# Kernel tuning notes

Measured on AMD Instinct MI355X. Metric: run time of the kernel, lower is better.

Reference implementation:

```python
import jax, jax.numpy as jnp
import numpy as np
import math

D_MODEL = 1024
N_HEADS = 16
D_HEAD = 64
GROUP_SIZE = 2
N_GROUPS = N_HEADS // GROUP_SIZE
D_MLP = 4096
BATCH = 2
SEQ = 2048
LN_EPS = 1e-5


def setup_inputs() -> dict:
    key = jax.random.key(0)
    ks = jax.random.split(key, 12)

    def xavier(k, shape):
        # torch xavier_uniform on a 3D tensor treats dim0 as fan_in, prod(rest) as fan_out
        fan_in = shape[0]
        fan_out = int(np.prod(shape[1:]))
        bound = math.sqrt(6.0 / (fan_in + fan_out))
        return jax.random.uniform(k, shape, jnp.float32, -bound, bound)

    def linear_w(k, out_f, in_f):
        bound = 1.0 / math.sqrt(in_f)
        return jax.random.uniform(k, (out_f, in_f), jnp.float32, -bound, bound)

    return {
        "x": jax.random.normal(ks[0], (BATCH, SEQ, D_MODEL), jnp.float32),
        "ln1_w": jnp.ones((D_MODEL,), jnp.float32),
        "ln1_b": jnp.zeros((D_MODEL,), jnp.float32),
        "W_Q": xavier(ks[1], (D_MODEL, N_HEADS, D_HEAD)),
        "W_K": xavier(ks[2], (D_MODEL, N_GROUPS, D_HEAD)),
        "W_V": xavier(ks[3], (D_MODEL, N_GROUPS, D_HEAD)),
        "W_out": xavier(ks[4], (D_HEAD, N_HEADS, D_MODEL)),
        "b_out": jnp.zeros((D_MODEL,), jnp.float32),
        "ln2_w": jnp.ones((D_MODEL,), jnp.float32),
        "ln2_b": jnp.zeros((D_MODEL,), jnp.float32),
        "mlp1_w": linear_w(ks[5], D_MLP, D_MODEL),
        "mlp1_b": jax.random.uniform(ks[6], (D_MLP,), jnp.float32, -1.0 / math.sqrt(D_MODEL), 1.0 / math.sqrt(D_MODEL)),
        "mlp2_w": linear_w(ks[7], D_MODEL, D_MLP),
        "mlp2_b": jax.random.uniform(ks[8], (D_MODEL,), jnp.float32, -1.0 / math.sqrt(D_MLP), 1.0 / math.sqrt(D_MLP)),
    }


def _layernorm(x, w, b):
    mu = jnp.mean(x, axis=-1, keepdims=True)
    var = jnp.var(x, axis=-1, keepdims=True)
    return (x - mu) * jax.lax.rsqrt(var + LN_EPS) * w + b


def _gqa_attention(resid, W_Q, W_K, W_V, W_out, b_out):
    b, s, _ = resid.shape
    q = jnp.einsum("bsd,dhk->bshk", resid, W_Q)            # [b, s, n_heads, d_head]
    q = q.reshape(b, s, N_GROUPS, GROUP_SIZE, D_HEAD)      # [b, s, g, gs, k]
    k = jnp.einsum("bsd,dgk->bsgk", resid, W_K)            # [b, s, g, k]
    v = jnp.einsum("bsd,dgk->bsgk", resid, W_V)
    scores = jnp.einsum("bqgik,btgk->bgiqt", q, k) / math.sqrt(D_HEAD)  # [b, g, gs, q, t]
    causal_mask = jnp.triu(jnp.ones((s, s), dtype=bool), k=1)
    scores = jnp.where(causal_mask, jnp.float32(-1000000.0), scores)
    probs = jax.nn.softmax(scores, axis=-1)
    z = jnp.einsum("bgiqt,btgk->bqgik", probs, v)          # [b, q, g, gs, k]
    z = z.reshape(b, s, N_HEADS, D_HEAD)
    return jnp.einsum("bshk,khd->bsd", z, W_out) + b_out


def reference(x, ln1_w, ln1_b, W_Q, W_K, W_V, W_out, b_out,
              ln2_w, ln2_b, mlp1_w, mlp1_b, mlp2_w, mlp2_b):
    normed = _layernorm(x, ln1_w, ln1_b)
    attn_out = _gqa_attention(normed, W_Q, W_K, W_V, W_out, b_out)
    post_attn = x + attn_out
    h = _layernorm(post_attn, ln2_w, ln2_b)
    h = jax.nn.gelu(h @ mlp1_w.T + mlp1_b, approximate=False)  # torch nn.GELU default = exact erf
    mlp_out = h @ mlp2_w.T + mlp2_b
    return post_attn + mlp_out
```

## Files before the change

kernel.cpp:

```cpp
#include <hip/hip_runtime.h>
#include <cstdint>
#include <cstddef>

typedef __attribute__((ext_vector_type(8))) short short8;
typedef __attribute__((ext_vector_type(4))) float f32x4;
typedef unsigned short u16;

#define MFMA16(a, b, c) __builtin_amdgcn_mfma_f32_16x16x32_bf16((a), (b), (c), 0, 0, 0)
#define SCL2 0.18033688011112042f

__device__ __forceinline__ u16 f2bf(float f) {
  union { float f; unsigned u; } c; c.f = f;
  unsigned r = c.u + 0x7fffu + ((c.u >> 16) & 1u);
  return (u16)(r >> 16);
}

__device__ __forceinline__ float bf2f(u16 x) {
  union { unsigned u; float f; } c; c.u = ((unsigned)x) << 16;
  return c.f;
}

__device__ __forceinline__ unsigned cvtpk(float a, float b) {
  unsigned r;
  asm("v_cvt_pk_bf16_f32 %0, %1, %2" : "=v"(r) : "v"(a), "v"(b));
  return r;
}


__global__ __launch_bounds__(256) void prep_wqkv(const float* __restrict__ wq,
    const float* __restrict__ wk, const float* __restrict__ wv, u16* __restrict__ outp)
{
  __shared__ float t[32][33];
  const int tx = threadIdx.x & 31, ty = threadIdx.x >> 5;
  const int n0 = blockIdx.x * 32, d0 = blockIdx.y * 32;
  const float* src; int stride, nc;
  if (n0 < 1024)      { src = wq; stride = 1024; nc = n0; }
  else if (n0 < 1536) { src = wk; stride = 512;  nc = n0 - 1024; }
  else                { src = wv; stride = 512;  nc = n0 - 1536; }
#pragma unroll
  for (int i = 0; i < 32; i += 8)
    t[ty + i][tx] = src[(size_t)(d0 + ty + i) * stride + nc + tx];
  __syncthreads();
#pragma unroll
  for (int i = 0; i < 32; i += 8)
    outp[(size_t)(n0 + ty + i) * 1024 + d0 + tx] = f2bf(t[tx][ty + i]);
}

__global__ __launch_bounds__(256) void prep_wout(const float* __restrict__ wo, u16* __restrict__ outp)
{
  __shared__ float t[32][33];
  const int tx = threadIdx.x & 31, ty = threadIdx.x >> 5;
  const int d0 = blockIdx.x * 32, c0 = blockIdx.y * 32;
#pragma unroll
  for (int i = 0; i < 32; i += 8) {
    int c = c0 + ty + i;
    t[ty + i][tx] = wo[(size_t)(c & 63) * 16384 + (size_t)(c >> 6) * 1024 + d0 + tx];
  }
  __syncthreads();
#pragma unroll
  for (int i = 0; i < 32; i += 8)
    outp[(size_t)(d0 + ty + i) * 1024 + c0 + tx] = f2bf(t[tx][ty + i]);
}

__global__ void convert_bf16(const float4* __restrict__ in, u16* __restrict__ out, int n4) {
  int i = blockIdx.x * 256 + threadIdx.x;
  if (i >= n4) return;
  float4 v = in[i];
  ushort4 o; o.x = f2bf(v.x); o.y = f2bf(v.y); o.z = f2bf(v.z); o.w = f2bf(v.w);
  ((ushort4*)out)[i] = o;
}

__global__ __launch_bounds__(256) void vt_transpose(const u16* __restrict__ qkv, u16* __restrict__ vtp)
{
  __shared__ u16 t[32][33];
  const int tx = threadIdx.x & 31, ty = threadIdx.x >> 5;
  const int t0 = blockIdx.x * 32, k0 = blockIdx.y * 32;
  const int bg = blockIdx.z, b = bg >> 3, g = bg & 7;
#pragma unroll
  for (int i = 0; i < 32; i += 8)
    t[ty + i][tx] = qkv[(size_t)(b * 2048 + t0 + ty + i) * 2048 + 1536 + g * 64 + k0 + tx];
  __syncthreads();
#pragma unroll
  for (int i = 0; i < 32; i += 8)
    vtp[(size_t)(bg * 64 + k0 + ty + i) * 2048 + t0 + tx] = t[tx][ty + i];
}

__global__ __launch_bounds__(256) void ln_bf16(const float* __restrict__ x,
    const float* __restrict__ w, const float* __restrict__ b, u16* __restrict__ out)
{
  const int row = blockIdx.x, tid = threadIdx.x;
  const float4 v = ((const float4*)(x + (size_t)row * 1024))[tid];
  float s = v.x + v.y + v.z + v.w;
  float s2 = v.x * v.x + v.y * v.y + v.z * v.z + v.w * v.w;
#pragma unroll
  for (int m = 32; m >= 1; m >>= 1) { s += __shfl_xor(s, m); s2 += __shfl_xor(s2, m); }
  __shared__ float red[8];
  if ((tid & 63) == 0) { red[tid >> 6] = s; red[4 + (tid >> 6)] = s2; }
  __syncthreads();
  s  = red[0] + red[1] + red[2] + red[3];
  s2 = red[4] + red[5] + red[6] + red[7];
  const float mu = s * (1.f / 1024.f);
  const float inv = rsqrtf(s2 * (1.f / 1024.f) - mu * mu + 1e-5f);
  const float4 wv = ((const float4*)w)[tid];
  const float4 bv = ((const float4*)b)[tid];
  ushort4 o;
  o.x = f2bf((v.x - mu) * inv * wv.x + bv.x);
  o.y = f2bf((v.y - mu) * inv * wv.y + bv.y);
  o.z = f2bf((v.z - mu) * inv * wv.z + bv.z);
  o.w = f2bf((v.w - mu) * inv * wv.w + bv.w);
  ((ushort4*)out)[(size_t)row * 256 + tid] = o;
}

#define BM 128
#define BN 128
#define BK 32

template<int EPI>
__global__ __launch_bounds__(256, 2) void gemm_bt(
    const u16* __restrict__ A, const u16* __restrict__ Bt, void* __restrict__ Cout,
    const float* __restrict__ bias, const float* __restrict__ resid,
    int M, int N, int K)
{
  __shared__ u16 As[4][BM * BK];
  __shared__ u16 Bs[4][BN * BK];
  const int tid = threadIdx.x;
  const int w = tid >> 6, lane = tid & 63;
  const int lo = lane & 15, hi = lane >> 4;
  const int mBase = blockIdx.x * BM, nBase = blockIdx.y * BN;
  const int wr = (w >> 1) * 64, wc = (w & 1) * 64;

  const f32x4 vzero = {0.f, 0.f, 0.f, 0.f};
  f32x4 acc[4][4];
#pragma unroll
  for (int i = 0; i < 4; ++i)
#pragma unroll
    for (int j = 0; j < 4; ++j) acc[i][j] = vzero;

  const int base0 = w * 2048 + lane * 16;
  int srow[2], skb[2];
#pragma unroll
  for (int c = 0; c < 2; ++c) {
    const int off = base0 + c * 1024;
    srow[c] = off >> 6;
    skb[c] = ((off & 63) ^ ((srow[c] & 3) << 4)) >> 1;
  }

  const int NT = K >> 5;

  auto stage = [&](int kt) {
    const int slot = kt & 3;
    const int k0 = kt * BK;
#pragma unroll
    for (int c = 0; c < 2; ++c) {
      const u16* ga = A  + (size_t)(mBase + srow[c]) * K + k0 + skb[c];
      const u16* gb = Bt + (size_t)(nBase + srow[c]) * K + k0 + skb[c];
      __builtin_amdgcn_global_load_lds((const __attribute__((address_space(1))) void*)ga,
          (__attribute__((address_space(3))) void*)((char*)&As[slot][0] + w * 2048 + c * 1024), 16, 0, 0);
      __builtin_amdgcn_global_load_lds((const __attribute__((address_space(1))) void*)gb,
          (__attribute__((address_space(3))) void*)((char*)&Bs[slot][0] + w * 2048 + c * 1024), 16, 0, 0);
    }
  };

  stage(0);
  stage(1);

  for (int kt = 0; kt < NT; ++kt) {
    if (kt + 2 < NT) {
      stage(kt + 2);
      asm volatile("s_waitcnt vmcnt(8)" ::: "memory");
    } else if (kt + 1 < NT) {
      asm volatile("s_waitcnt vmcnt(4)" ::: "memory");
    } else {
      asm volatile("s_waitcnt vmcnt(0)" ::: "memory");
    }
    __builtin_amdgcn_s_barrier();
    __builtin_amdgcn_sched_barrier(0);

    const int slot = kt & 3;
    short8 af[4], bf[4];
#pragma unroll
    for (int i = 0; i < 4; ++i) {
      const int ra = wr + i * 16 + lo;
      const int rb = wc + i * 16 + lo;
      af[i] = *(const short8*)((const char*)&As[slot][0] + ra * 64 + ((hi * 16) ^ ((ra & 3) << 4)));
      bf[i] = *(const short8*)((const char*)&Bs[slot][0] + rb * 64 + ((hi * 16) ^ ((rb & 3) << 4)));
    }
    __builtin_amdgcn_s_setprio(1);
#pragma unroll
    for (int i = 0; i < 4; ++i)
#pragma unroll
      for (int j = 0; j < 4; ++j)
        acc[i][j] = MFMA16(af[i], bf[j], acc[i][j]);
    __builtin_amdgcn_s_setprio(0);
  }

#pragma unroll
  for (int i = 0; i < 4; ++i) {
#pragma unroll
    for (int j = 0; j < 4; ++j) {
#pragma unroll
      for (int r = 0; r < 4; ++r) {
        const int row = mBase + wr + i * 16 + hi * 4 + r;
        const int col = nBase + wc + j * 16 + lo;
        float v = acc[i][j][r];
        if (EPI == 3 && col < 1024) v *= SCL2;
        ((u16*)Cout)[(size_t)row * N + col] = f2bf(v);
      }
    }
  }
}

template<int EPI>
__global__ __launch_bounds__(256, 3) void gemm_n64(
    const u16* __restrict__ A, const u16* __restrict__ Bt, void* __restrict__ Cout,
    const float* __restrict__ bias, const float* __restrict__ resid,
    int M, int N, int K)
{
  __shared__ u16 As[4][128 * 32];
  __shared__ u16 Bs[4][64 * 32];
  const int tid = threadIdx.x;
  const int w = tid >> 6, lane = tid & 63;
  const int lo = lane & 15, hi = lane >> 4;
  const int mBase = blockIdx.x * 128, nBase = blockIdx.y * 64;
  const int wr = (w >> 1) * 64, wc = (w & 1) * 32;

  const f32x4 vzero = {0.f, 0.f, 0.f, 0.f};
  f32x4 acc[4][2];
#pragma unroll
  for (int i = 0; i < 4; ++i)
#pragma unroll
    for (int j = 0; j < 2; ++j) acc[i][j] = vzero;

  int arow[2], akb[2];
#pragma unroll
  for (int c = 0; c < 2; ++c) {
    const int off = tid * 16 + c * 4096;
    arow[c] = off >> 6;
    akb[c] = ((off & 63) ^ ((arow[c] & 3) << 4)) >> 1;
  }
  const int boff = tid * 16;
  const int brow = boff >> 6;
  const int bkb = ((boff & 63) ^ ((brow & 3) << 4)) >> 1;

  const int NT = K >> 5;

  auto stage = [&](int kt) {
    const int slot = kt & 3;
    const int k0 = kt * 32;
#pragma unroll
    for (int c = 0; c < 2; ++c) {
      const u16* ga = A + (size_t)(mBase + arow[c]) * K + k0 + akb[c];
      __builtin_amdgcn_global_load_lds((const __attribute__((address_space(1))) void*)ga,
          (__attribute__((address_space(3))) void*)((char*)&As[slot][0] + tid * 16 + c * 4096), 16, 0, 0);
    }
    const u16* gb = Bt + (size_t)(nBase + brow) * K + k0 + bkb;
    __builtin_amdgcn_global_load_lds((const __attribute__((address_space(1))) void*)gb,
        (__attribute__((address_space(3))) void*)((char*)&Bs[slot][0] + tid * 16), 16, 0, 0);
  };

  stage(0);
  stage(1);

  for (int kt = 0; kt < NT; ++kt) {
    if (kt + 2 < NT) {
      stage(kt + 2);
      asm volatile("s_waitcnt vmcnt(6)" ::: "memory");
    } else if (kt + 1 < NT) {
      asm volatile("s_waitcnt vmcnt(3)" ::: "memory");
    } else {
      asm volatile("s_waitcnt vmcnt(0)" ::: "memory");
    }
    __builtin_amdgcn_s_barrier();
    __builtin_amdgcn_sched_barrier(0);

    const int slot = kt & 3;
    short8 af[4], bf[2];
#pragma unroll
    for (int i = 0; i < 4; ++i) {
      const int ra = wr + i * 16 + lo;
      af[i] = *(const short8*)((const char*)&As[slot][0] + ra * 64 + ((hi * 16) ^ ((ra & 3) << 4)));
    }
#pragma unroll
    for (int j = 0; j < 2; ++j) {
      const int rb = wc + j * 16 + lo;
      bf[j] = *(const short8*)((const char*)&Bs[slot][0] + rb * 64 + ((hi * 16) ^ ((rb & 3) << 4)));
    }
    __builtin_amdgcn_s_setprio(1);
#pragma unroll
    for (int i = 0; i < 4; ++i)
#pragma unroll
      for (int j = 0; j < 2; ++j)
        acc[i][j] = MFMA16(af[i], bf[j], acc[i][j]);
    __builtin_amdgcn_s_setprio(0);
  }

#pragma unroll
  for (int i = 0; i < 4; ++i) {
#pragma unroll
    for (int j = 0; j < 2; ++j) {
#pragma unroll
      for (int r = 0; r < 4; ++r) {
        const int row = mBase + wr + i * 16 + hi * 4 + r;
        const int col = nBase + wc + j * 16 + lo;
        float v = acc[i][j][r];
        v += bias[col];
        v += resid[(size_t)row * N + col];
        ((float*)Cout)[(size_t)row * N + col] = v;
      }
    }
  }
}

template<int EPI>
__global__ __launch_bounds__(512, 2) void gemm256(
    const u16* __restrict__ A, const u16* __restrict__ Bt, void* __restrict__ Cout,
    const float* __restrict__ bias, const float* __restrict__ resid,
    int M, int N, int K)
{
  __shared__ u16 lds8[2][2][2][8192];
  const int tid = threadIdx.x;
  const int lane = tid & 63, lo = lane & 15, hi = lane >> 4;
  const int wid = tid >> 6, wr = wid >> 2, wc = wid & 3;
  const int mBase = blockIdx.x * 256, nBase = blockIdx.y * 256;
  const int sw = (lo & 7) << 4;

  const f32x4 vzero = {0.f, 0.f, 0.f, 0.f};
  f32x4 acc[8][4];
#pragma unroll
  for (int i = 0; i < 8; ++i)
#pragma unroll
    for (int j = 0; j < 4; ++j) acc[i][j] = vzero;

  int srow[2], scol[2];
#pragma unroll
  for (int c = 0; c < 2; ++c) {
    const int p = c * 8192 + tid * 16;
    const int r = p >> 7, bb = p & 127;
    srow[c] = r;
    scol[c] = (bb ^ ((r & 7) << 4)) >> 1;
  }

  const int NT = K >> 6;

#pragma unroll
  for (int mat = 0; mat < 2; ++mat)
#pragma unroll
    for (int half = 0; half < 2; ++half)
#pragma unroll
      for (int c = 0; c < 2; ++c) {
        const u16* g = (mat == 0)
          ? A  + (size_t)(mBase + half * 128 + srow[c]) * K + scol[c]
          : Bt + (size_t)(nBase + half * 128 + srow[c]) * K + scol[c];
        __builtin_amdgcn_global_load_lds((const __attribute__((address_space(1))) void*)g,
            (__attribute__((address_space(3))) void*)(&lds8[0][mat][half][c * 4096 + tid * 8]), 16, 0, 0);
      }
  asm volatile("s_waitcnt vmcnt(0)" ::: "memory");
  asm volatile("s_barrier" ::: "memory");

  for (int kt = 0; kt < NT; ++kt) {
    const int cur = kt & 1;
    const char* baseA = (const char*)&lds8[cur][0][wr][0];
    const char* baseB = (const char*)&lds8[cur][1][wc >> 1][0];
    const int rBB = (wc & 1) * 64;

    short8 bfr[4][2], afr[4][2];
#pragma unroll
    for (int nf = 0; nf < 4; ++nf)
#pragma unroll
      for (int ks = 0; ks < 2; ++ks)
        bfr[nf][ks] = *(const short8*)(baseB + (rBB + nf * 16 + lo) * 128 + ((ks * 64 + hi * 16) ^ sw));
#pragma unroll
    for (int mf = 0; mf < 4; ++mf)
#pragma unroll
      for (int ks = 0; ks < 2; ++ks)
        afr[mf][ks] = *(const short8*)(baseA + ((mf * 16 + lo) * 128 + ((ks * 64 + hi * 16) ^ sw)));

    if (kt + 1 < NT) {
      const int ko = (kt + 1) * 64;
#pragma unroll
      for (int mat = 0; mat < 2; ++mat)
#pragma unroll
        for (int half = 0; half < 2; ++half)
#pragma unroll
          for (int c = 0; c < 2; ++c) {
            const u16* g = (mat == 0)
              ? A  + (size_t)(mBase + half * 128 + srow[c]) * K + ko + scol[c]
              : Bt + (size_t)(nBase + half * 128 + srow[c]) * K + ko + scol[c];
            __builtin_amdgcn_global_load_lds((const __attribute__((address_space(1))) void*)g,
                (__attribute__((address_space(3))) void*)(&lds8[cur ^ 1][mat][half][c * 4096 + tid * 8]), 16, 0, 0);
          }
    }

    __builtin_amdgcn_s_setprio(1);
#pragma unroll
    for (int mf = 0; mf < 4; ++mf)
#pragma unroll
      for (int nf = 0; nf < 4; ++nf)
#pragma unroll
        for (int ks = 0; ks < 2; ++ks)
          acc[mf][nf] = MFMA16(afr[mf][ks], bfr[nf][ks], acc[mf][nf]);
    __builtin_amdgcn_s_setprio(0);

#pragma unroll
    for (int mf = 0; mf < 4; ++mf)
#pragma unroll
      for (int ks = 0; ks < 2; ++ks)
        afr[mf][ks] = *(const short8*)(baseA + (((mf + 4) * 16 + lo) * 128 + ((ks * 64 + hi * 16) ^ sw)));

    __builtin_amdgcn_s_setprio(1);
#pragma unroll
    for (int mf = 0; mf < 4; ++mf)
#pragma unroll
      for (int nf = 0; nf < 4; ++nf)
#pragma unroll
        for (int ks = 0; ks < 2; ++ks)
          acc[mf + 4][nf] = MFMA16(afr[mf][ks], bfr[nf][ks], acc[mf + 4][nf]);
    __builtin_amdgcn_s_setprio(0);

    asm volatile("s_waitcnt vmcnt(0)" ::: "memory");
    asm volatile("s_barrier" ::: "memory");
  }

#pragma unroll
  for (int mf = 0; mf < 8; ++mf) {
#pragma unroll
    for (int nf = 0; nf < 4; ++nf) {
#pragma unroll
      for (int r = 0; r < 4; ++r) {
        const int row = mBase + wr * 128 + mf * 16 + hi * 4 + r;
        const int col = nBase + wc * 64 + nf * 16 + lo;
        float v = acc[mf][nf][r];
        if (EPI != 0) v += bias[col];
        if (EPI == 1) v += resid[(size_t)row * N + col];
        if (EPI == 2) v = 0.5f * v * (1.f + erff(v * 0.70710678118f));
        if (EPI == 1) ((float*)Cout)[(size_t)row * N + col] = v;
        else          ((u16*)Cout)[(size_t)row * N + col] = f2bf(v);
      }
    }
  }
}

__global__ __launch_bounds__(256) void attn_fwd(const u16* __restrict__ qkv,
    const u16* __restrict__ vt, u16* __restrict__ z,
    u16* __restrict__ zscr, float* __restrict__ lscr)
{
  __shared__ u16 Ks[2][64 * 64];
  __shared__ u16 Vs[2][64 * 64];
  __shared__ u16 Pl[4][32 * 72];
  const int tid = threadIdx.x;
  const int w = tid >> 6, lane = tid & 63, lo = lane & 15, hi = lane >> 4;
  const int bx = blockIdx.x;
  int chunk, itBeg, itEnd, mode;
  if (bx < 16)      { chunk = bx;      itBeg = 0;  itEnd = chunk + 1; mode = 0; }
  else if (bx < 32) { chunk = bx;      itBeg = 0;  itEnd = 16;        mode = 1; }
  else              { chunk = bx - 16; itBeg = 16; itEnd = chunk + 1; mode = 2; }
  const int bg = blockIdx.y, b = bg >> 3, g = bg & 7;
  const int h = (g << 1) | (w & 1);
  const int q0w = chunk * 64 + (w >> 1) * 32;
  const int sw = (lo & 7) << 4;

  short8 qA[2][2];
#pragma unroll
  for (int qf = 0; qf < 2; ++qf)
#pragma unroll
    for (int half = 0; half < 2; ++half)
      qA[qf][half] = *(const short8*)(qkv +
          (size_t)(b * 2048 + q0w + qf * 16 + lo) * 2048 + h * 64 + half * 32 + hi * 8);

  const f32x4 vzero = {0.f, 0.f, 0.f, 0.f};
  f32x4 zacc[2][4];
#pragma unroll
  for (int qf = 0; qf < 2; ++qf)
#pragma unroll
    for (int kf = 0; kf < 4; ++kf) zacc[qf][kf] = vzero;
  float lrun[2] = {0.f, 0.f};

  const u16* kbase = qkv + (size_t)b * 2048 * 2048 + 1024 + g * 64;
  const u16* vbase = vt + (size_t)(b * 8 + g) * 64 * 2048;

  int srow[2], scol[2];
#pragma unroll
  for (int c = 0; c < 2; ++c) {
    const int p = tid * 16 + c * 4096;
    const int r = p >> 7, bb = p & 127;
    srow[c] = r;
    scol[c] = (bb ^ ((r & 7) << 4)) >> 1;
  }

  u16* pw = &Pl[w][0];

  auto stageKV = [&](int it) {
    const int slot = it & 1;
    const int t0 = it * 64;
#pragma unroll
    for (int c = 0; c < 2; ++c) {
      __builtin_amdgcn_global_load_lds(
          (const __attribute__((address_space(1))) void*)(kbase + (size_t)(t0 + srow[c]) * 2048 + scol[c]),
          (__attribute__((address_space(3))) void*)((char*)&Ks[slot][0] + tid * 16 + c * 4096), 16, 0, 0);
      __builtin_amdgcn_global_load_lds(
          (const __attribute__((address_space(1))) void*)(vbase + (size_t)srow[c] * 2048 + t0 + scol[c]),
          (__attribute__((address_space(3))) void*)((char*)&Vs[slot][0] + tid * 16 + c * 4096), 16, 0, 0);
    }
  };

  stageKV(itBeg);

  for (int it = itBeg; it < itEnd; ++it) {
    asm volatile("s_waitcnt vmcnt(0)" ::: "memory");
    __builtin_amdgcn_s_barrier();
    __builtin_amdgcn_sched_barrier(0);
    if (it + 1 < itEnd) stageKV(it + 1);

    const int slot = it & 1;
    const int ts = it * 64;
    const char* KsB = (const char*)&Ks[slot][0];
    const char* VsB = (const char*)&Vs[slot][0];

    short8 kA[4][2];
#pragma unroll
    for (int nt = 0; nt < 4; ++nt)
#pragma unroll
      for (int half = 0; half < 2; ++half)
        kA[nt][half] = *(const short8*)(KsB + (nt * 16 + lo) * 128 + ((half * 64 + hi * 16) ^ sw));

#pragma unroll
    for (int qf = 0; qf < 2; ++qf) {
      f32x4 p[4];
#pragma unroll
      for (int nt = 0; nt < 4; ++nt) {
        f32x4 t = MFMA16(kA[nt][0], qA[qf][0], vzero);
        p[nt] = MFMA16(kA[nt][1], qA[qf][1], t);
      }
      const int qrow0 = q0w + qf * 16;
      if (ts + 63 > qrow0) {
        const int rel = qrow0 + lo - ts;
#pragma unroll
        for (int nt = 0; nt < 4; ++nt)
#pragma unroll
          for (int r = 0; r < 4; ++r)
            if (nt * 16 + hi * 4 + r > rel) p[nt][r] = -1e30f;
      }
#pragma unroll
      for (int nt = 0; nt < 4; ++nt)
#pragma unroll
        for (int r = 0; r < 4; ++r) p[nt][r] = exp2f(p[nt][r]);
      float s0 = (p[0][0] + p[0][1]) + (p[0][2] + p[0][3]);
      float s1 = (p[1][0] + p[1][1]) + (p[1][2] + p[1][3]);
      float s2 = (p[2][0] + p[2][1]) + (p[2][2] + p[2][3]);
      float s3 = (p[3][0] + p[3][1]) + (p[3][2] + p[3][3]);
      lrun[qf] += (s0 + s1) + (s2 + s3);
#pragma unroll
      for (int nt = 0; nt < 4; ++nt) {
        uint2 uu;
        uu.x = cvtpk(p[nt][0], p[nt][1]);
        uu.y = cvtpk(p[nt][2], p[nt][3]);
        *(uint2*)((char*)pw + (qf * 16 + lo) * 144 + nt * 32 + hi * 8) = uu;
      }
    }
    asm volatile("s_waitcnt lgkmcnt(0)" ::: "memory");
    short8 pa[2][2];
#pragma unroll
    for (int qf = 0; qf < 2; ++qf)
#pragma unroll
      for (int tc = 0; tc < 2; ++tc)
        pa[qf][tc] = *(const short8*)((const char*)pw + (qf * 16 + lo) * 144 + tc * 64 + hi * 16);
#pragma unroll
    for (int kf = 0; kf < 4; ++kf) {
#pragma unroll
      for (int tc = 0; tc < 2; ++tc) {
        const short8 vf = *(const short8*)(VsB + (kf * 16 + lo) * 128 + ((tc * 64 + hi * 16) ^ sw));
        zacc[0][kf] = MFMA16(vf, pa[0][tc], zacc[0][kf]);
        zacc[1][kf] = MFMA16(vf, pa[1][tc], zacc[1][kf]);
      }
    }
  }

  if (mode == 0) {
    u16* zp = z + (size_t)(b * 2048 + q0w) * 1024 + h * 64;
#pragma unroll
    for (int qf = 0; qf < 2; ++qf) {
      float rs = lrun[qf];
      rs += __shfl_xor(rs, 16);
      rs += __shfl_xor(rs, 32);
      const float inv = 1.f / rs;
#pragma unroll
      for (int kf = 0; kf < 4; ++kf) {
        uint2 o;
        o.x = cvtpk(zacc[qf][kf][0] * inv, zacc[qf][kf][1] * inv);
        o.y = cvtpk(zacc[qf][kf][2] * inv, zacc[qf][kf][3] * inv);
        *(uint2*)(zp + (size_t)(qf * 16 + lo) * 1024 + kf * 16 + hi * 4) = o;
      }
    }
  } else {
    const int seg = mode - 1;
    const int ci = chunk - 16;
    const int idx2 = (bg * 16 + ci) * 2 + (w & 1);
    u16* zs = zscr + ((size_t)seg * 512 * 4096) + ((size_t)idx2 * 64 + (w >> 1) * 32) * 64;
    float* ls = lscr + (size_t)seg * 512 * 64 + (size_t)idx2 * 64 + (w >> 1) * 32;
#pragma unroll
    for (int qf = 0; qf < 2; ++qf) {
      float rs = lrun[qf];
      rs += __shfl_xor(rs, 16);
      rs += __shfl_xor(rs, 32);
      if (hi == 0) ls[qf * 16 + lo] = rs;
#pragma unroll
      for (int kf = 0; kf < 4; ++kf) {
        uint2 o;
        o.x = cvtpk(zacc[qf][kf][0], zacc[qf][kf][1]);
        o.y = cvtpk(zacc[qf][kf][2], zacc[qf][kf][3]);
        *(uint2*)(zs + (size_t)(qf * 16 + lo) * 64 + kf * 16 + hi * 4) = o;
      }
    }
  }
}

__global__ __launch_bounds__(256) void attn_combine(const u16* __restrict__ zscr,
    const float* __restrict__ lscr, u16* __restrict__ z)
{
  const int bgci = blockIdx.x;
  const int bg = bgci >> 4, ci = bgci & 15;
  const int b = bg >> 3, g = bg & 7, chunk = 16 + ci;
  const int tid = threadIdx.x;
#pragma unroll
  for (int j = 0; j < 4; ++j) {
    const int v = tid + j * 256;
    const int k8 = v & 7, row = (v >> 3) & 63, hh = v >> 9;
    const size_t base = ((size_t)(bgci * 2 + hh) * 64 + row) * 64 + k8 * 8;
    const short8 z0 = *(const short8*)(zscr + base);
    const short8 z1 = *(const short8*)(zscr + (size_t)512 * 4096 + base);
    const size_t lidx = (size_t)(bgci * 2 + hh) * 64 + row;
    const float inv = 1.f / (lscr[lidx] + lscr[(size_t)512 * 64 + lidx]);
    float a[8];
#pragma unroll
    for (int e = 0; e < 8; ++e)
      a[e] = (bf2f((u16)z0[e]) + bf2f((u16)z1[e])) * inv;
    uint4 o;
    o.x = cvtpk(a[0], a[1]);
    o.y = cvtpk(a[2], a[3]);
    o.z = cvtpk(a[4], a[5]);
    o.w = cvtpk(a[6], a[7]);
    *(uint4*)(z + ((size_t)(b * 2048 + chunk * 64 + row)) * 1024 + (g * 2 + hh) * 64 + k8 * 8) = o;
  }
}


extern "C" void kernel_launch(void* const* d_in, const int* in_sizes, int n_in,
                              void* d_out, int out_size, void* d_ws, size_t ws_size,
                              hipStream_t stream)
{
  (void)in_sizes; (void)n_in; (void)out_size; (void)ws_size;
  const float* x      = (const float*)d_in[0];
  const float* ln1_w  = (const float*)d_in[1];
  const float* ln1_b  = (const float*)d_in[2];
  const float* W_Q    = (const float*)d_in[3];
  const float* W_K    = (const float*)d_in[4];
  const float* W_V    = (const float*)d_in[5];
  const float* W_out  = (const float*)d_in[6];
  const float* b_out  = (const float*)d_in[7];
  const float* ln2_w  = (const float*)d_in[8];
  const float* ln2_b  = (const float*)d_in[9];
  const float* mlp1_w = (const float*)d_in[10];
  const float* mlp1_b = (const float*)d_in[11];
  const float* mlp2_w = (const float*)d_in[12];
  const float* mlp2_b = (const float*)d_in[13];
  float* out = (float*)d_out;

  char* ws = (char*)d_ws;
  u16*   wqkv_t = (u16*)(ws + 0);
  u16*   wout_t = (u16*)(ws + 4194304);
  u16*   w1     = (u16*)(ws + 6291456);
  u16*   w2     = (u16*)(ws + 14680064);
  u16*   normed = (u16*)(ws + 23068672);
  float* post   = (float*)(ws + 31457280);
  u16*   qkv    = (u16*)(ws + 48234496);
  u16*   vtb    = (u16*)(ws + 65011712);
  u16*   zb     = (u16*)(ws + 69206016);
  u16*   hbuf   = (u16*)(ws + 48234496);
  u16*   zscr   = (u16*)(ws + 31457280);
  float* lscr   = (float*)(ws + 23068672);

  prep_wqkv<<<dim3(64, 32), 256, 0, stream>>>(W_Q, W_K, W_V, wqkv_t);
  prep_wout<<<dim3(32, 32), 256, 0, stream>>>(W_out, wout_t);
  convert_bf16<<<4096, 256, 0, stream>>>((const float4*)mlp1_w, w1, 1048576);
  convert_bf16<<<4096, 256, 0, stream>>>((const float4*)mlp2_w, w2, 1048576);

  ln_bf16<<<4096, 256, 0, stream>>>(x, ln1_w, ln1_b, normed);
  gemm_bt<3><<<dim3(32, 16), 256, 0, stream>>>(normed, wqkv_t, qkv, nullptr, nullptr, 4096, 2048, 1024);
  vt_transpose<<<dim3(64, 2, 16), 256, 0, stream>>>(qkv, vtb);
  attn_fwd<<<dim3(48, 16), 256, 0, stream>>>(qkv, vtb, zb, zscr, lscr);
  attn_combine<<<256, 256, 0, stream>>>(zscr, lscr, zb);
  gemm_n64<1><<<dim3(32, 16), 256, 0, stream>>>(zb, wout_t, post, b_out, x, 4096, 1024, 1024);
  ln_bf16<<<4096, 256, 0, stream>>>(post, ln2_w, ln2_b, normed);
  gemm256<2><<<dim3(16, 16), 512, 0, stream>>>(normed, w1, hbuf, mlp1_b, nullptr, 4096, 4096, 1024);
  gemm_n64<1><<<dim3(32, 16), 256, 0, stream>>>(hbuf, w2, out, mlp2_b, post, 4096, 1024, 4096);
}
```

Before: 248.7 us.

## Split-K the MLP down-projection across two partial GEMMs plus combine kernel

Replaces the N=64-tile gemm for the second MLP matmul with the 128x128 gemm_bt kernel run as split-K over blockIdx.z. Each half writes bf16 partial sums to scratch, and a new combine kernel adds the partials, bias and residual into the fp32 output. The goal is larger tiles with more blocks (512 instead of 256 as 128x128) and better reuse. The cost is an extra launch, partial-sum traffic and bf16 rounding of the partials. The gemm_n64 template is also de-templated, and its attention out-projection launch now drops the <1> argument.

```diff
diff --git a/kernel.cpp b/kernel.cpp
--- a/kernel.cpp
+++ b/kernel.cpp
@@ -117,9 +117,10 @@
 
 template<int EPI>
 __global__ __launch_bounds__(256, 2) void gemm_bt(
-    const u16* __restrict__ A, const u16* __restrict__ Bt, void* __restrict__ Cout,
+    const u16* __restrict__ A, const u16* __restrict__ Bt,
+    void* __restrict__ Cout, void* __restrict__ Cout2,
     const float* __restrict__ bias, const float* __restrict__ resid,
-    int M, int N, int K)
+    int M, int N, int K, int Ks)
 {
   __shared__ u16 As[4][BM * BK];
   __shared__ u16 Bs[4][BN * BK];
@@ -128,6 +129,8 @@
   const int lo = lane & 15, hi = lane >> 4;
   const int mBase = blockIdx.x * BM, nBase = blockIdx.y * BN;
   const int wr = (w >> 1) * 64, wc = (w & 1) * 64;
+  A += (size_t)blockIdx.z * K;
+  Bt += (size_t)blockIdx.z * K;
 
   const f32x4 vzero = {0.f, 0.f, 0.f, 0.f};
   f32x4 acc[4][4];
@@ -152,8 +155,8 @@
     const int k0 = kt * BK;
 #pragma unroll
     for (int c = 0; c < 2; ++c) {
-      const u16* ga = A  + (size_t)(mBase + srow[c]) * K + k0 + skb[c];
-      const u16* gb = Bt + (size_t)(nBase + srow[c]) * K + k0 + skb[c];
+      const u16* ga = A  + (size_t)(mBase + srow[c]) * Ks + k0 + skb[c];
+      const u16* gb = Bt + (size_t)(nBase + srow[c]) * Ks + k0 + skb[c];
       __builtin_amdgcn_global_load_lds((const __attribute__((address_space(1))) void*)ga,
           (__attribute__((address_space(3))) void*)((char*)&As[slot][0] + w * 2048 + c * 1024), 16, 0, 0);
       __builtin_amdgcn_global_load_lds((const __attribute__((address_space(1))) void*)gb,
@@ -194,6 +197,7 @@
     __builtin_amdgcn_s_setprio(0);
   }
 
+  void* sel = (EPI == 4 && blockIdx.z) ? Cout2 : Cout;
 #pragma unroll
   for (int i = 0; i < 4; ++i) {
 #pragma unroll
@@ -204,13 +208,35 @@
         const int col = nBase + wc + j * 16 + lo;
         float v = acc[i][j][r];
         if (EPI == 3 && col < 1024) v *= SCL2;
-        ((u16*)Cout)[(size_t)row * N + col] = f2bf(v);
-      }
-    }
-  }
-}
-
-template<int EPI>
+        ((u16*)sel)[(size_t)row * N + col] = f2bf(v);
+      }
+    }
+  }
+}
+
+__global__ __launch_bounds__(256) void mlp2_combine(const u16* __restrict__ p0,
+    const u16* __restrict__ p1, const float* __restrict__ bias,
+    const float* __restrict__ resid, float* __restrict__ out)
+{
+  const int tid = threadIdx.x;
+  const int c0 = tid * 4;
+  const float4 bv = *(const float4*)(bias + c0);
+#pragma unroll
+  for (int rr = 0; rr < 4; ++rr) {
+    const int row = blockIdx.x * 4 + rr;
+    const size_t off = (size_t)row * 1024 + c0;
+    const ushort4 a = *(const ushort4*)(p0 + off);
+    const ushort4 b = *(const ushort4*)(p1 + off);
+    const float4 rv = *(const float4*)(resid + off);
+    float4 o;
+    o.x = bf2f(a.x) + bf2f(b.x) + bv.x + rv.x;
+    o.y = bf2f(a.y) + bf2f(b.y) + bv.y + rv.y;
+    o.z = bf2f(a.z) + bf2f(b.z) + bv.z + rv.z;
+    o.w = bf2f(a.w) + bf2f(b.w) + bv.w + rv.w;
+    *(float4*)(out + off) = o;
+  }
+}
+
 __global__ __launch_bounds__(256, 3) void gemm_n64(
     const u16* __restrict__ A, const u16* __restrict__ Bt, void* __restrict__ Cout,
     const float* __restrict__ bias, const float* __restrict__ resid,
@@ -678,6 +704,8 @@
   u16*   hbuf   = (u16*)(ws + 48234496);
   u16*   zscr   = (u16*)(ws + 31457280);
   float* lscr   = (float*)(ws + 23068672);
+  u16*   mp0    = (u16*)(ws + 0);
+  u16*   mp1    = (u16*)(ws + 23068672);
 
   prep_wqkv<<<dim3(64, 32), 256, 0, stream>>>(W_Q, W_K, W_V, wqkv_t);
   prep_wout<<<dim3(32, 32), 256, 0, stream>>>(W_out, wout_t);
@@ -685,12 +713,13 @@
   convert_bf16<<<4096, 256, 0, stream>>>((const float4*)mlp2_w, w2, 1048576);
 
   ln_bf16<<<4096, 256, 0, stream>>>(x, ln1_w, ln1_b, normed);
-  gemm_bt<3><<<dim3(32, 16), 256, 0, stream>>>(normed, wqkv_t, qkv, nullptr, nullptr, 4096, 2048, 1024);
+  gemm_bt<3><<<dim3(32, 16), 256, 0, stream>>>(normed, wqkv_t, qkv, nullptr, nullptr, nullptr, 4096, 2048, 1024, 1024);
   vt_transpose<<<dim3(64, 2, 16), 256, 0, stream>>>(qkv, vtb);
   attn_fwd<<<dim3(48, 16), 256, 0, stream>>>(qkv, vtb, zb, zscr, lscr);
   attn_combine<<<256, 256, 0, stream>>>(zscr, lscr, zb);
-  gemm_n64<1><<<dim3(32, 16), 256, 0, stream>>>(zb, wout_t, post, b_out, x, 4096, 1024, 1024);
+  gemm_n64<<<dim3(32, 16), 256, 0, stream>>>(zb, wout_t, post, b_out, x, 4096, 1024, 1024);
   ln_bf16<<<4096, 256, 0, stream>>>(post, ln2_w, ln2_b, normed);
   gemm256<2><<<dim3(16, 16), 512, 0, stream>>>(normed, w1, hbuf, mlp1_b, nullptr, 4096, 4096, 1024);
-  gemm_n64<1><<<dim3(32, 16), 256, 0, stream>>>(hbuf, w2, out, mlp2_b, post, 4096, 1024, 4096);
-}
+  gemm_bt<4><<<dim3(32, 8, 2), 256, 0, stream>>>(hbuf, w2, mp0, mp1, nullptr, nullptr, 4096, 1024, 2048, 4096);
+  mlp2_combine<<<1024, 256, 0, stream>>>(mp0, mp1, mlp2_b, post, out);
+}
```

Result: faster. 241.9 us, median of 5 (-2.7%).
